# Kernel tuning notes

Hardware: AMD Instinct MI355X
Metric: run time of the kernel (lower is better)

Reference implementation:

```python
import jax, jax.numpy as jnp
import numpy as np

N_NODES = 100000
N_EDGES = 1600000
EPS = 1e-12  # F.normalize eps


def _lin(key, i, o):
    return jax.random.normal(key, (i, o), jnp.float32) * 0.05


def setup_inputs() -> dict:
    key = jax.random.key(0)
    ks = jax.random.split(key, 16)
    inp = {
        'x': jax.random.normal(ks[0], (N_NODES, 100), jnp.float32),
        'edge_index': jax.random.randint(ks[1], (2, N_EDGES), 0, N_NODES, dtype=jnp.int64),
        'edge_weight': jax.random.uniform(ks[2], (N_EDGES,), jnp.float32),
        'emb_W': _lin(ks[3], 100, 80), 'emb_b': jnp.zeros((80,), jnp.float32),
        'Wl0': _lin(ks[4], 80, 64), 'Wr0': _lin(ks[5], 80, 64), 'b0': jnp.zeros((64,), jnp.float32),
        'Wl1': _lin(ks[6], 64, 64), 'Wr1': _lin(ks[7], 64, 64), 'b1': jnp.zeros((64,), jnp.float32),
        'Wl2': _lin(ks[8], 64, 64), 'Wr2': _lin(ks[9], 64, 64), 'b2': jnp.zeros((64,), jnp.float32),
        'Wl3': _lin(ks[10], 64, 64), 'Wr3': _lin(ks[11], 64, 64), 'b3': jnp.zeros((64,), jnp.float32),
        'Wlo': _lin(ks[12], 64, 18), 'Wro': _lin(ks[13], 64, 18), 'bo': jnp.zeros((18,), jnp.float32),
    }
    return inp


def _sage_conv(x, src, dst, ew, Wl, Wr, b):
    # message: edge_weight * x_j, mean-aggregated onto dst nodes
    msg = x[src] * ew[:, None]                                   # [E, C]
    agg = jax.ops.segment_sum(msg, dst, num_segments=N_NODES)    # [N, C]
    deg = jax.ops.segment_sum(jnp.ones_like(ew), dst, num_segments=N_NODES)
    agg = agg / jnp.maximum(deg, 1.0)[:, None]
    out = agg @ Wl + x @ Wr + b
    nrm = jnp.linalg.norm(out, axis=-1, keepdims=True)
    return out / jnp.maximum(nrm, EPS)                           # L2 normalize


def reference(x, edge_index, edge_weight, emb_W, emb_b,
              Wl0, Wr0, b0, Wl1, Wr1, b1, Wl2, Wr2, b2, Wl3, Wr3, b3,
              Wlo, Wro, bo):
    src, dst = edge_index[0], edge_index[1]
    h = jax.nn.relu(x @ emb_W + emb_b)                           # embedding
    ones_w = jnp.ones_like(edge_weight)
    for Wl, Wr, b in ((Wl0, Wr0, b0), (Wl1, Wr1, b1), (Wl2, Wr2, b2), (Wl3, Wr3, b3)):
        h = _sage_conv(h, src, dst, edge_weight, Wl, Wr, b)
        h = jax.nn.relu(h)
        # dropout(p=0.2) is identity in eval mode
    h = _sage_conv(h, src, dst, ones_w, Wlo, Wro, bo)            # out layer (no edge_weight)
    return h
```

## Files before the change

### kernel.cpp

```cpp
#include <hip/hip_runtime.h>
#include <hip/hip_bf16.h>

#define N_NODES 100000
#define N_EDGES 1600000
#define SCAN_BLOCKS ((N_NODES+255)/256)

using bf16 = __hip_bfloat16;
typedef unsigned int u32;
typedef __attribute__((ext_vector_type(8))) short short8;
typedef __attribute__((ext_vector_type(4))) float f32x4;

static __device__ __forceinline__ float b2f(bf16 v){ return __bfloat162float(v); }

static __device__ __forceinline__ float ldf(const void* p, long i, int f32m){
  return f32m ? ((const float*)p)[i] : b2f(((const bf16*)p)[i]);
}

static __device__ __forceinline__ u32 f2bf_rne(float f){
  u32 b = __float_as_uint(f);
  return (b + 0x7fffu + ((b>>16)&1u)) >> 16;
}

__global__ void k_detect(const u32* __restrict__ xw, const int* __restrict__ eiw,
                         int* __restrict__ flags){
  __shared__ int s_wild, s_nzodd;
  if(threadIdx.x==0){ s_wild=0; s_nzodd=0; }
  __syncthreads();
  int wild=0, nz=0;
  for(int k=threadIdx.x;k<2048;k+=256){
    u32 w  = xw[k];
    u32 lo = w & 0xffffu;
    int e  = (int)((lo>>7)&0xffu);
    if((lo & 0x7fffu)!=0u && (e<90 || e>160)) wild++;
    if(eiw[2*k+1]!=0) nz++;
  }
  atomicAdd(&s_wild, wild);
  atomicAdd(&s_nzodd, nz);
  __syncthreads();
  if(threadIdx.x==0){
    flags[0] = (s_wild > 512) ? 1 : 0;
    flags[1] = (s_nzodd == 0) ? 1 : 0;
  }
}

__global__ void k_zero2(int* __restrict__ a, int* __restrict__ b){
  int i = blockIdx.x*256 + threadIdx.x;
  if(i<N_NODES){ a[i]=0; b[i]=0; }
}

__global__ void k_cvt(const void* __restrict__ W, const void* __restrict__ b,
                      const int* __restrict__ flags, float* __restrict__ Wo,
                      float* __restrict__ bo_){
  int i = blockIdx.x*256 + threadIdx.x;
  int f32m = flags[0];
  if(i<8000) Wo[i] = ldf(W,i,f32m);
  if(i<80)   bo_[i] = ldf(b,i,f32m);
}


__global__ void k_count(const int* __restrict__ ei, const int* __restrict__ flags,
                        int* __restrict__ deg){
  int e = blockIdx.x*256 + threadIdx.x;
  int i64 = flags[1];
  if(e < N_EDGES){
    long di = i64 ? 2l*(N_EDGES + e) : (long)(N_EDGES + e);
    atomicAdd(&deg[ei[di]], 1);
  }
}

__global__ void k_scan1(const int* __restrict__ deg, int* __restrict__ off,
                        int* __restrict__ bsum){
  const int t = threadIdx.x, lane = t&63, wid = t>>6;
  const int i = blockIdx.x*256 + t;
  int v = (i<N_NODES) ? deg[i] : 0;
  const int orig = v;
  #pragma unroll
  for(int d=1; d<64; d<<=1){ int u = __shfl_up(v,d); if(lane>=d) v += u; }
  __shared__ int wsum[4];
  if(lane==63) wsum[wid] = v;
  __syncthreads();
  int wbase = 0;
  for(int k=0;k<wid;k++) wbase += wsum[k];
  if(i<N_NODES) off[i] = wbase + v - orig;
  if(t==255) bsum[blockIdx.x] = wbase + v;
}

__global__ void k_scan2(const int* __restrict__ bsum, int* __restrict__ bbase){
  const int t = threadIdx.x, lane = t&63, wid = t>>6;
  int v = (t<SCAN_BLOCKS) ? bsum[t] : 0;
  const int orig = v;
  #pragma unroll
  for(int d=1; d<64; d<<=1){ int u = __shfl_up(v,d); if(lane>=d) v += u; }
  __shared__ int wsum[8];
  if(lane==63) wsum[wid] = v;
  __syncthreads();
  int wbase = 0;
  for(int k=0;k<wid;k++) wbase += wsum[k];
  if(t<SCAN_BLOCKS) bbase[t] = wbase + v - orig;
}

__global__ void k_scan3(int* __restrict__ off, const int* __restrict__ bbase){
  const int i = blockIdx.x*256 + threadIdx.x;
  if(i<N_NODES) off[i] += bbase[blockIdx.x];
  if(i==0) off[N_NODES] = N_EDGES;
}

__global__ void k_fill(const int* __restrict__ ei, const void* __restrict__ ew,
                       const int* __restrict__ flags, const int* __restrict__ off,
                       int* __restrict__ cur, uint2* __restrict__ csr){
  const int xcd = blockIdx.x & 7;
  const int e = (blockIdx.x>>3)*256 + threadIdx.x;
  const int i64 = flags[1], f32m = flags[0];
  if(e < N_EDGES){
    int d = ei[i64 ? 2l*(N_EDGES+e) : (long)(N_EDGES+e)];
    if(d/12500 == xcd){
      int s = ei[i64 ? 2l*e : (long)e];
      int p = atomicAdd(&cur[d], 1);
      csr[off[d]+p] = make_uint2((u32)s, __float_as_uint(ldf(ew, e, f32m)));
    }
  }
}


__global__ void k_packb(const void* __restrict__ Wl, const void* __restrict__ Wr,
                        const int* __restrict__ flags, int CIN, int COUT,
                        int KT, int NT, short* __restrict__ out){
  int idx = blockIdx.x*256 + threadIdx.x;
  int total = KT*NT*512;
  if(idx < total){
    int jj = idx & 7;
    int l  = (idx>>3) & 63;
    int tile = idx >> 9;
    int nt = tile % NT, kt = tile / NT;
    int k   = kt*32 + ((l>>4)<<3) + jj;
    int col = nt*16 + (l&15);
    int khalf = (KT/2)*32;
    float v = 0.f;
    if(col < COUT){
      int f32m = flags[0];
      if(k < khalf){ if(k < CIN) v = ldf(Wl,(long)k*COUT+col,f32m); }
      else { int ch = k - khalf; if(ch < CIN) v = ldf(Wr,(long)ch*COUT+col,f32m); }
    }
    out[idx] = (short)f2bf_rne(v);
  }
}


__global__ __launch_bounds__(256) void k_embed(const void* __restrict__ x,
                                               const float* __restrict__ W,
                                               const float* __restrict__ b,
                                               const int* __restrict__ flags,
                                               bf16* __restrict__ h){
  __shared__ float xs[100][65];
  const int t = threadIdx.x;
  const int n0 = blockIdx.x*64;
  if(flags[0]){
    const float* xf = (const float*)x;
    for(int idx=t; idx<1600; idx+=256){
      int n = idx/25, q = idx-25*(idx/25);
      float4 v = (n0+n < N_NODES) ? *(const float4*)(xf + (long)(n0+n)*100 + 4*q)
                                  : make_float4(0.f,0.f,0.f,0.f);
      xs[4*q+0][n]=v.x; xs[4*q+1][n]=v.y; xs[4*q+2][n]=v.z; xs[4*q+3][n]=v.w;
    }
  } else {
    const u32* xu = (const u32*)x;
    for(int idx=t; idx<3200; idx+=256){
      int n = idx/50, q = idx-50*(idx/50);
      u32 v = (n0+n < N_NODES) ? xu[(long)(n0+n)*50 + q] : 0u;
      xs[2*q+0][n]=__uint_as_float(v<<16);
      xs[2*q+1][n]=__uint_as_float(v&0xffff0000u);
    }
  }
  __syncthreads();

  const int ng = t&15, og = t>>4;
  float acc[4][5];
  #pragma unroll
  for(int j=0;j<5;j++){
    float bj = b[og*5+j];
    #pragma unroll
    for(int i=0;i<4;i++) acc[i][j] = bj;
  }
  #pragma unroll 2
  for(int c=0;c<100;c++){
    float xv[4];
    #pragma unroll
    for(int i=0;i<4;i++) xv[i] = xs[c][ng*4+i];
    #pragma unroll
    for(int j=0;j<5;j++){
      float wj = W[c*80+og*5+j];
      #pragma unroll
      for(int i=0;i<4;i++) acc[i][j] = fmaf(xv[i], wj, acc[i][j]);
    }
  }
  #pragma unroll
  for(int i=0;i<4;i++){
    int n = n0 + ng*4 + i;
    if(n < N_NODES){
      #pragma unroll
      for(int j=0;j<5;j++)
        h[(long)n*80 + og*5+j] = __float2bfloat16(fmaxf(acc[i][j], 0.f));
    }
  }
}


template<int CIN, int COUT, bool LAST>
__global__ __launch_bounds__(128,6) void k_sage(
    const void* __restrict__ hin, const int* __restrict__ off,
    const uint2* __restrict__ csr,
    const short* __restrict__ Wb, const void* __restrict__ bias,
    const int* __restrict__ flags, bf16* __restrict__ hout, void* __restrict__ outp)
{
  constexpr int RB   = CIN*2;
  constexpr int KHT  = (CIN+31)/32;
  constexpr int KT   = 2*KHT;
  constexpr int NT   = (COUT+15)/16;
  constexpr int ROWB = KT*32*2;
  constexpr int LPE  = CIN/8;
  constexpr int EPW  = 64/LPE;

  __shared__ char smem[2*16*ROWB];

  const int f32m = flags[0];
  const int lane = threadIdx.x&63, wid = threadIdx.x>>6;
  const int wnode0 = blockIdx.x*32 + wid*16;
  char* lds = smem + wid*16*ROWB;

  const int sub = lane/LPE;
  const int cl  = lane - sub*LPE;
  const bool lact = (sub < EPW);
  const char* hinb = (const char*)hin;

  for(int tt=0; tt<16; ++tt){
    const int node = wnode0 + tt;
    if(node >= N_NODES) continue;

    float a[8];
    #pragma unroll
    for(int k=0;k<8;k++) a[k]=0.f;

    const int e0 = off[node], e1 = off[node+1];
    for(int base=e0; base<e1; base+=64){
      const int cnt = min(64, e1-base);
      uint2 ev = (lane<cnt) ? csr[base+lane] : make_uint2(0u,0u);
      int   sv = (int)ev.x;
      float wv = LAST ? 1.f : __uint_as_float(ev.y);
      for(int j=0; j<cnt; j+=4*EPW){
        int ei0 = j+sub, ei1 = j+EPW+sub, ei2 = j+2*EPW+sub, ei3 = j+3*EPW+sub;
        bool v0 = lact && (ei0<cnt), v1 = lact && (ei1<cnt);
        bool v2 = lact && (ei2<cnt), v3 = lact && (ei3<cnt);
        int x0 = v0?ei0:0, x1 = v1?ei1:0, x2 = v2?ei2:0, x3 = v3?ei3:0;
        int   s0=__shfl(sv,x0), s1=__shfl(sv,x1), s2=__shfl(sv,x2), s3=__shfl(sv,x3);
        float w0=__shfl(wv,x0)*(v0?1.f:0.f), w1=__shfl(wv,x1)*(v1?1.f:0.f);
        float w2=__shfl(wv,x2)*(v2?1.f:0.f), w3=__shfl(wv,x3)*(v3?1.f:0.f);
        uint4 r0 = *(const uint4*)(hinb + (long)s0*RB + 16*cl);
        uint4 r1 = *(const uint4*)(hinb + (long)s1*RB + 16*cl);
        uint4 r2 = *(const uint4*)(hinb + (long)s2*RB + 16*cl);
        uint4 r3 = *(const uint4*)(hinb + (long)s3*RB + 16*cl);
        #define ACC8(rr,ww) \
          a[0]=fmaf(ww,__uint_as_float(rr.x<<16),a[0]); \
          a[1]=fmaf(ww,__uint_as_float(rr.x&0xffff0000u),a[1]); \
          a[2]=fmaf(ww,__uint_as_float(rr.y<<16),a[2]); \
          a[3]=fmaf(ww,__uint_as_float(rr.y&0xffff0000u),a[3]); \
          a[4]=fmaf(ww,__uint_as_float(rr.z<<16),a[4]); \
          a[5]=fmaf(ww,__uint_as_float(rr.z&0xffff0000u),a[5]); \
          a[6]=fmaf(ww,__uint_as_float(rr.w<<16),a[6]); \
          a[7]=fmaf(ww,__uint_as_float(rr.w&0xffff0000u),a[7]);
        ACC8(r0,w0); ACC8(r1,w1); ACC8(r2,w2); ACC8(r3,w3);
        #undef ACC8
      }
    }

    if(LPE==8){
      #pragma unroll
      for(int k=0;k<8;k++){
        a[k]+=__shfl_xor(a[k],8); a[k]+=__shfl_xor(a[k],16); a[k]+=__shfl_xor(a[k],32);
      }
    } else {
      #pragma unroll
      for(int k=0;k<8;k++){
        a[k] = __shfl(a[k],cl)    + __shfl(a[k],cl+10) + __shfl(a[k],cl+20)
             + __shfl(a[k],cl+30) + __shfl(a[k],cl+40) + __shfl(a[k],cl+50);
      }
    }
    const float inv = 1.f/fmaxf((float)(e1-e0), 1.f);

    const int sx = (tt&7)<<4;
    if(lane < LPE){
      u32 p0 = f2bf_rne(a[0]*inv) | (f2bf_rne(a[1]*inv)<<16);
      u32 p1 = f2bf_rne(a[2]*inv) | (f2bf_rne(a[3]*inv)<<16);
      u32 p2 = f2bf_rne(a[4]*inv) | (f2bf_rne(a[5]*inv)<<16);
      u32 p3 = f2bf_rne(a[6]*inv) | (f2bf_rne(a[7]*inv)<<16);
      int ob = tt*ROWB + lane*16;
      *(uint4*)(lds + (ob^sx)) = make_uint4(p0,p1,p2,p3);
    }
    if(CIN==80 && lane>=10 && lane<12){
      int ob = tt*ROWB + lane*16;
      *(uint4*)(lds + (ob^sx)) = make_uint4(0u,0u,0u,0u);
    }
    const char* hsb = hinb + (long)__builtin_amdgcn_readfirstlane(node)*RB;
    if(lane < RB/16){
      uint4 hv = *(const uint4*)(hsb + lane*16);
      int ob = tt*ROWB + KHT*64 + lane*16;
      *(uint4*)(lds + (ob^sx)) = hv;
    }
    if(CIN==80 && lane>=20 && lane<22){
      int ob = tt*ROWB + KHT*64 + (lane-10)*16;
      *(uint4*)(lds + (ob^sx)) = make_uint4(0u,0u,0u,0u);
    }
  }

  f32x4 acc[NT];
  #pragma unroll
  for(int nt=0; nt<NT; ++nt){
    int col = nt*16 + (lane&15);
    float bv = (col<COUT) ? ldf(bias,col,f32m) : 0.f;
    acc[nt] = (f32x4){bv,bv,bv,bv};
  }
  const int arow = lane&15, kgrp = lane>>4;
  #pragma unroll
  for(int kt=0; kt<KT; ++kt){
    int ob = arow*ROWB + kt*64 + kgrp*16;
    short8 a8 = *(const short8*)(lds + (ob ^ ((arow&7)<<4)));
    #pragma unroll
    for(int nt=0; nt<NT; ++nt){
      short8 b8 = *(const short8*)(Wb + ((long)(kt*NT+nt)*64 + lane)*8);
      acc[nt] = __builtin_amdgcn_mfma_f32_16x16x32_bf16(a8, b8, acc[nt], 0,0,0);
    }
  }

  float sq[4];
  #pragma unroll
  for(int r=0;r<4;r++){
    float s = 0.f;
    #pragma unroll
    for(int nt=0;nt<NT;nt++){ float v = acc[nt][r]; s = fmaf(v,v,s); }
    #pragma unroll
    for(int d=1; d<16; d<<=1) s += __shfl_xor(s, d);
    sq[r] = s;
  }
  #pragma unroll
  for(int r=0;r<4;r++){
    float rn = 1.f/fmaxf(sqrtf(sq[r]), 1e-12f);
    const int node = wnode0 + 4*(lane>>4) + r;
    #pragma unroll
    for(int nt=0;nt<NT;nt++){
      int col = nt*16 + (lane&15);
      float v = acc[nt][r]*rn;
      if(!LAST) v = fmaxf(v,0.f);
      if(node < N_NODES && col < COUT){
        if(LAST){
          long oi = (long)node*COUT + col;
          if(f32m) ((float*)outp)[oi] = v;
          else     ((bf16*)outp)[oi]  = __float2bfloat16(v);
        } else {
          hout[(long)node*64 + col] = __float2bfloat16(v);
        }
      }
    }
  }
}


extern "C" void kernel_launch(void* const* d_in, const int* in_sizes, int n_in,
                              void* d_out, int out_size, void* d_ws, size_t ws_size,
                              hipStream_t stream){
  const void* x    = d_in[0];
  const int*  ei   = (const int*)d_in[1];
  const void* ew   = d_in[2];
  const void* embW = d_in[3];
  const void* embB = d_in[4];
  const void *Wl0=d_in[5],  *Wr0=d_in[6],  *b0=d_in[7];
  const void *Wl1=d_in[8],  *Wr1=d_in[9],  *b1=d_in[10];
  const void *Wl2=d_in[11], *Wr2=d_in[12], *b2=d_in[13];
  const void *Wl3=d_in[14], *Wr3=d_in[15], *b3=d_in[16];
  const void *Wlo=d_in[17], *Wro=d_in[18], *bo=d_in[19];

  char* w = (char*)d_ws;
  auto carve = [&](size_t nbytes)->char*{
    char* r = w; w += (nbytes + 255) & ~(size_t)255; return r;
  };
  int*   flags   = (int*)carve(16);
  int*   deg     = (int*)carve((size_t)N_NODES*4);
  int*   cur     = (int*)carve((size_t)N_NODES*4);
  int*   off     = (int*)carve((size_t)(N_NODES+1)*4);
  int*   bsum    = (int*)carve((size_t)SCAN_BLOCKS*4);
  int*   bbase   = (int*)carve((size_t)SCAN_BLOCKS*4);
  uint2* csr     = (uint2*)carve((size_t)N_EDGES*8);
  short* Wb0     = (short*)carve((size_t)6*4*512*2);
  short* Wb1     = (short*)carve((size_t)4*4*512*2);
  short* Wb2     = (short*)carve((size_t)4*4*512*2);
  short* Wb3     = (short*)carve((size_t)4*4*512*2);
  short* Wbo     = (short*)carve((size_t)4*2*512*2);
  float* Wef     = (float*)carve((size_t)8000*4);
  float* bef     = (float*)carve((size_t)80*4);
  bf16*  hE      = (bf16*)carve((size_t)N_NODES*80*2);
  bf16*  hA      = (bf16*)carve((size_t)N_NODES*64*2);
  bf16*  hB      = (bf16*)carve((size_t)N_NODES*64*2);

  k_detect<<<1, 256, 0, stream>>>((const u32*)x, ei, flags);
  k_zero2<<<(N_NODES+255)/256, 256, 0, stream>>>(deg, cur);
  k_count<<<N_EDGES/256, 256, 0, stream>>>(ei, flags, deg);
  k_scan1<<<SCAN_BLOCKS, 256, 0, stream>>>(deg, off, bsum);
  k_scan2<<<1, 512, 0, stream>>>(bsum, bbase);
  k_scan3<<<SCAN_BLOCKS, 256, 0, stream>>>(off, bbase);
  k_fill <<<8*(N_EDGES/256), 256, 0, stream>>>(ei, ew, flags, off, cur, csr);

  k_cvt  <<<32, 256, 0, stream>>>(embW, embB, flags, Wef, bef);
  k_packb<<<48, 256, 0, stream>>>(Wl0, Wr0, flags, 80, 64, 6, 4, Wb0);
  k_packb<<<32, 256, 0, stream>>>(Wl1, Wr1, flags, 64, 64, 4, 4, Wb1);
  k_packb<<<32, 256, 0, stream>>>(Wl2, Wr2, flags, 64, 64, 4, 4, Wb2);
  k_packb<<<32, 256, 0, stream>>>(Wl3, Wr3, flags, 64, 64, 4, 4, Wb3);
  k_packb<<<16, 256, 0, stream>>>(Wlo, Wro, flags, 64, 18, 4, 2, Wbo);

  k_embed<<<(N_NODES+63)/64, 256, 0, stream>>>(x, Wef, bef, flags, hE);

  const int NBLK = (N_NODES+31)/32;
  k_sage<80,64,false><<<NBLK, 128, 0, stream>>>(hE, off, csr, Wb0, b0, flags, hA, nullptr);
  k_sage<64,64,false><<<NBLK, 128, 0, stream>>>(hA, off, csr, Wb1, b1, flags, hB, nullptr);
  k_sage<64,64,false><<<NBLK, 128, 0, stream>>>(hB, off, csr, Wb2, b2, flags, hA, nullptr);
  k_sage<64,64,false><<<NBLK, 128, 0, stream>>>(hA, off, csr, Wb3, b3, flags, hB, nullptr);
  k_sage<64,18,true ><<<NBLK, 128, 0, stream>>>(hB, off, csr, Wbo, bo, flags, nullptr, d_out);
}
```

Before: 524.5 us.

## Sort nodes by in-degree and assign degree-strided groups to waves for balance

Adds a degree-histogram counting sort (hist, scan, scatter) that builds a node permutation ordered by in-degree. Each SAGE wave then processes 16 nodes taken at stride NWAVE through this permutation, so every wave gets a similar mix of degrees instead of 16 consecutive nodes. The goal is to even out per-wave gather work and cut tail imbalance. It costs three small extra kernels, an extra perm lookup per node, and scattered output writes with less locality. It also relies on N_NODES being divisible by 16 and drops the bounds check.

```diff
diff --git a/kernel.cpp b/kernel.cpp
--- a/kernel.cpp
+++ b/kernel.cpp
@@ -4,6 +4,7 @@
 #define N_NODES 100000
 #define N_EDGES 1600000
 #define SCAN_BLOCKS ((N_NODES+255)/256)
+#define NWAVE (N_NODES/16)
 
 using bf16 = __hip_bfloat16;
 typedef unsigned int u32;
@@ -43,9 +44,11 @@
   }
 }
 
-__global__ void k_zero2(int* __restrict__ a, int* __restrict__ b){
+__global__ void k_zero2(int* __restrict__ a, int* __restrict__ b,
+                        int* __restrict__ hist){
   int i = blockIdx.x*256 + threadIdx.x;
   if(i<N_NODES){ a[i]=0; b[i]=0; }
+  if(blockIdx.x==0 && threadIdx.x<256) hist[threadIdx.x]=0;
 }
 
 __global__ void k_cvt(const void* __restrict__ W, const void* __restrict__ b,
@@ -118,6 +121,35 @@
       int p = atomicAdd(&cur[d], 1);
       csr[off[d]+p] = make_uint2((u32)s, __float_as_uint(ldf(ew, e, f32m)));
     }
+  }
+}
+
+
+__global__ void k_hist(const int* __restrict__ deg, int* __restrict__ hist){
+  int i = blockIdx.x*256 + threadIdx.x;
+  if(i<N_NODES) atomicAdd(&hist[min(deg[i],255)], 1);
+}
+
+__global__ void k_hscan(const int* __restrict__ hist, int* __restrict__ hcur){
+  const int t = threadIdx.x, lane = t&63, wid = t>>6;
+  int v = hist[t];
+  const int orig = v;
+  #pragma unroll
+  for(int d=1; d<64; d<<=1){ int u = __shfl_up(v,d); if(lane>=d) v += u; }
+  __shared__ int wsum[4];
+  if(lane==63) wsum[wid] = v;
+  __syncthreads();
+  int wbase = 0;
+  for(int k=0;k<wid;k++) wbase += wsum[k];
+  hcur[t] = wbase + v - orig;
+}
+
+__global__ void k_scatter(const int* __restrict__ deg, int* __restrict__ hcur,
+                          int* __restrict__ perm){
+  int i = blockIdx.x*256 + threadIdx.x;
+  if(i<N_NODES){
+    int pos = atomicAdd(&hcur[min(deg[i],255)], 1);
+    perm[pos] = i;
   }
 }
 
@@ -208,7 +240,7 @@
 template<int CIN, int COUT, bool LAST>
 __global__ __launch_bounds__(128,6) void k_sage(
     const void* __restrict__ hin, const int* __restrict__ off,
-    const uint2* __restrict__ csr,
+    const uint2* __restrict__ csr, const int* __restrict__ perm,
     const short* __restrict__ Wb, const void* __restrict__ bias,
     const int* __restrict__ flags, bf16* __restrict__ hout, void* __restrict__ outp)
 {
@@ -224,7 +256,7 @@
 
   const int f32m = flags[0];
   const int lane = threadIdx.x&63, wid = threadIdx.x>>6;
-  const int wnode0 = blockIdx.x*32 + wid*16;
+  const int widx = blockIdx.x*2 + wid;
   char* lds = smem + wid*16*ROWB;
 
   const int sub = lane/LPE;
@@ -233,14 +265,24 @@
   const char* hinb = (const char*)hin;
 
   for(int tt=0; tt<16; ++tt){
-    const int node = wnode0 + tt;
-    if(node >= N_NODES) continue;
+    const int node = perm[widx + tt*NWAVE];
 
     float a[8];
     #pragma unroll
     for(int k=0;k<8;k++) a[k]=0.f;
 
     const int e0 = off[node], e1 = off[node+1];
+
+    #define ACC8(rr,ww) \
+      a[0]=fmaf(ww,__uint_as_float(rr.x<<16),a[0]); \
+      a[1]=fmaf(ww,__uint_as_float(rr.x&0xffff0000u),a[1]); \
+      a[2]=fmaf(ww,__uint_as_float(rr.y<<16),a[2]); \
+      a[3]=fmaf(ww,__uint_as_float(rr.y&0xffff0000u),a[3]); \
+      a[4]=fmaf(ww,__uint_as_float(rr.z<<16),a[4]); \
+      a[5]=fmaf(ww,__uint_as_float(rr.z&0xffff0000u),a[5]); \
+      a[6]=fmaf(ww,__uint_as_float(rr.w<<16),a[6]); \
+      a[7]=fmaf(ww,__uint_as_float(rr.w&0xffff0000u),a[7]);
+
     for(int base=e0; base<e1; base+=64){
       const int cnt = min(64, e1-base);
       uint2 ev = (lane<cnt) ? csr[base+lane] : make_uint2(0u,0u);
@@ -258,19 +300,10 @@
         uint4 r1 = *(const uint4*)(hinb + (long)s1*RB + 16*cl);
         uint4 r2 = *(const uint4*)(hinb + (long)s2*RB + 16*cl);
         uint4 r3 = *(const uint4*)(hinb + (long)s3*RB + 16*cl);
-        #define ACC8(rr,ww) \
-          a[0]=fmaf(ww,__uint_as_float(rr.x<<16),a[0]); \
-          a[1]=fmaf(ww,__uint_as_float(rr.x&0xffff0000u),a[1]); \
-          a[2]=fmaf(ww,__uint_as_float(rr.y<<16),a[2]); \
-          a[3]=fmaf(ww,__uint_as_float(rr.y&0xffff0000u),a[3]); \
-          a[4]=fmaf(ww,__uint_as_float(rr.z<<16),a[4]); \
-          a[5]=fmaf(ww,__uint_as_float(rr.z&0xffff0000u),a[5]); \
-          a[6]=fmaf(ww,__uint_as_float(rr.w<<16),a[6]); \
-          a[7]=fmaf(ww,__uint_as_float(rr.w&0xffff0000u),a[7]);
         ACC8(r0,w0); ACC8(r1,w1); ACC8(r2,w2); ACC8(r3,w3);
-        #undef ACC8
       }
     }
+    #undef ACC8
 
     if(LPE==8){
       #pragma unroll
@@ -343,13 +376,14 @@
   #pragma unroll
   for(int r=0;r<4;r++){
     float rn = 1.f/fmaxf(sqrtf(sq[r]), 1e-12f);
-    const int node = wnode0 + 4*(lane>>4) + r;
+    const int slot = 4*(lane>>4) + r;
+    const int node = perm[widx + slot*NWAVE];
     #pragma unroll
     for(int nt=0;nt<NT;nt++){
       int col = nt*16 + (lane&15);
       float v = acc[nt][r]*rn;
       if(!LAST) v = fmaxf(v,0.f);
-      if(node < N_NODES && col < COUT){
+      if(col < COUT){
         if(LAST){
           long oi = (long)node*COUT + col;
           if(f32m) ((float*)outp)[oi] = v;
@@ -387,6 +421,9 @@
   int*   off     = (int*)carve((size_t)(N_NODES+1)*4);
   int*   bsum    = (int*)carve((size_t)SCAN_BLOCKS*4);
   int*   bbase   = (int*)carve((size_t)SCAN_BLOCKS*4);
+  int*   hist    = (int*)carve((size_t)256*4);
+  int*   hcur    = (int*)carve((size_t)256*4);
+  int*   perm    = (int*)carve((size_t)N_NODES*4);
   uint2* csr     = (uint2*)carve((size_t)N_EDGES*8);
   short* Wb0     = (short*)carve((size_t)6*4*512*2);
   short* Wb1     = (short*)carve((size_t)4*4*512*2);
@@ -400,12 +437,16 @@
   bf16*  hB      = (bf16*)carve((size_t)N_NODES*64*2);
 
   k_detect<<<1, 256, 0, stream>>>((const u32*)x, ei, flags);
-  k_zero2<<<(N_NODES+255)/256, 256, 0, stream>>>(deg, cur);
+  k_zero2<<<(N_NODES+255)/256, 256, 0, stream>>>(deg, cur, hist);
   k_count<<<N_EDGES/256, 256, 0, stream>>>(ei, flags, deg);
   k_scan1<<<SCAN_BLOCKS, 256, 0, stream>>>(deg, off, bsum);
   k_scan2<<<1, 512, 0, stream>>>(bsum, bbase);
   k_scan3<<<SCAN_BLOCKS, 256, 0, stream>>>(off, bbase);
   k_fill <<<8*(N_EDGES/256), 256, 0, stream>>>(ei, ew, flags, off, cur, csr);
+
+  k_hist   <<<SCAN_BLOCKS, 256, 0, stream>>>(deg, hist);
+  k_hscan  <<<1, 256, 0, stream>>>(hist, hcur);
+  k_scatter<<<SCAN_BLOCKS, 256, 0, stream>>>(deg, hcur, perm);
 
   k_cvt  <<<32, 256, 0, stream>>>(embW, embB, flags, Wef, bef);
   k_packb<<<48, 256, 0, stream>>>(Wl0, Wr0, flags, 80, 64, 6, 4, Wb0);
@@ -416,10 +457,10 @@
 
   k_embed<<<(N_NODES+63)/64, 256, 0, stream>>>(x, Wef, bef, flags, hE);
 
-  const int NBLK = (N_NODES+31)/32;
-  k_sage<80,64,false><<<NBLK, 128, 0, stream>>>(hE, off, csr, Wb0, b0, flags, hA, nullptr);
-  k_sage<64,64,false><<<NBLK, 128, 0, stream>>>(hA, off, csr, Wb1, b1, flags, hB, nullptr);
-  k_sage<64,64,false><<<NBLK, 128, 0, stream>>>(hB, off, csr, Wb2, b2, flags, hA, nullptr);
-  k_sage<64,64,false><<<NBLK, 128, 0, stream>>>(hA, off, csr, Wb3, b3, flags, hB, nullptr);
-  k_sage<64,18,true ><<<NBLK, 128, 0, stream>>>(hB, off, csr, Wbo, bo, flags, nullptr, d_out);
-}
+  const int NBLK = NWAVE/2;
+  k_sage<80,64,false><<<NBLK, 128, 0, stream>>>(hE, off, csr, perm, Wb0, b0, flags, hA, nullptr);
+  k_sage<64,64,false><<<NBLK, 128, 0, stream>>>(hA, off, csr, perm, Wb1, b1, flags, hB, nullptr);
+  k_sage<64,64,false><<<NBLK, 128, 0, stream>>>(hB, off, csr, perm, Wb2, b2, flags, hA, nullptr);
+  k_sage<64,64,false><<<NBLK, 128, 0, stream>>>(hA, off, csr, perm, Wb3, b3, flags, hB, nullptr);
+  k_sage<64,18,true ><<<NBLK, 128, 0, stream>>>(hB, off, csr, perm, Wbo, bo, flags, nullptr, d_out);
+}
```

Result: slower. 1.127 ms (+114.8%).
